# Kernel tuning notes

Hardware: AMD Instinct MI355X
Metric: run time of the kernel (lower is better)

Reference implementation:

```python
import jax, jax.numpy as jnp
import numpy as np

# dims
B, S, LC, K, CE, L, WE, H = 64, 512, 16, 3, 10, 32, 200, 200
V, A, T = 50000, 128, 64
LP = LC + K - 1  # padded word length (pad_word adds (K-1)/2 on each side)
D_IN = WE + L    # LSTM input dim = 232


def setup_inputs() -> dict:
    key = jax.random.key(0)
    ks = jax.random.split(key, 16)
    f = lambda k, shp: jax.random.normal(k, shp, dtype=jnp.float32) * 0.05
    return {
        "char_ids": jax.random.randint(ks[0], (B, S, LP), 0, A),
        "word_ids": jax.random.randint(ks[1], (B, S), 0, V),
        "word_emb": f(ks[2], (V, WE)),
        "char_emb": f(ks[3], (A, CE)),
        "conv_w": f(ks[4], (L, K * CE)),   # Conv1d(1, l, K*CE) == linear 30->32
        "conv_b": f(ks[5], (L,)),
        "w_ih_f": f(ks[6], (4 * H, D_IN)),
        "w_hh_f": f(ks[7], (4 * H, H)),
        "b_ih_f": f(ks[8], (4 * H,)),
        "b_hh_f": f(ks[9], (4 * H,)),
        "w_ih_b": f(ks[10], (4 * H, D_IN)),
        "w_hh_b": f(ks[11], (4 * H, H)),
        "b_ih_b": f(ks[12], (4 * H,)),
        "b_hh_b": f(ks[13], (4 * H,)),
        "out_w": f(ks[14], (T, 2 * H)),
        "out_b": f(ks[15], (T,)),
    }


def _lstm(x, w_ih, w_hh, b_ih, b_hh, reverse):
    # x: [S, B, D]; PyTorch gate order i, f, g, o
    def step(carry, x_t):
        h, c = carry
        g = x_t @ w_ih.T + b_ih + h @ w_hh.T + b_hh
        i, f, gg, o = jnp.split(g, 4, axis=-1)
        c = jax.nn.sigmoid(f) * c + jax.nn.sigmoid(i) * jnp.tanh(gg)
        h = jax.nn.sigmoid(o) * jnp.tanh(c)
        return (h, c), h

    b = x.shape[1]
    init = (jnp.zeros((b, H), x.dtype), jnp.zeros((b, H), x.dtype))
    _, hs = jax.lax.scan(step, init, x, reverse=reverse)
    return hs  # [S, B, H]


def reference(char_ids, word_ids, word_emb, char_emb, conv_w, conv_b,
              w_ih_f, w_hh_f, b_ih_f, b_hh_f,
              w_ih_b, w_hh_b, b_ih_b, b_hh_b,
              out_w, out_b):
    # per-word char CNN + max-pool, fully batched over (B, S, windows)
    ce = char_emb[char_ids]                                    # [B,S,LP,CE]
    # sliding K-char windows, flattened to K*CE (== original x_hat construction)
    win = jnp.concatenate([ce[:, :, k:k + LC] for k in range(K)], axis=-1)  # [B,S,LC,K*CE]
    phi = jnp.einsum('bswd,ld->bswl', win, conv_w) + conv_b    # tiny conv == linear
    char_repr = phi.max(axis=2)                                # max-pool over positions -> [B,S,L]

    combined = jnp.concatenate([word_emb[word_ids], char_repr], axis=-1)  # [B,S,232]
    x = combined.reshape(S, B, D_IN)  # faithful to original .view (reshape, not transpose)

    hf = _lstm(x, w_ih_f, w_hh_f, b_ih_f, b_hh_f, reverse=False)
    hb = _lstm(x, w_ih_b, w_hh_b, b_ih_b, b_hh_b, reverse=True)
    lstm_out = jnp.concatenate([hf, hb], axis=-1)              # [S,B,2H]  (dropout: eval mode)

    tag_space = lstm_out.reshape(B, S, 2 * H) @ out_w.T + out_b  # faithful .view back
    return jax.nn.log_softmax(tag_space, axis=1)  # original normalizes over dim=1 (seq axis)
```

## Files before the change

kernel.cpp:

```cpp
#include <hip/hip_runtime.h>
#include <hip/hip_bf16.h>
#include <math.h>

constexpr int B_ = 64, S_ = 512, LP_ = 18, CE_ = 10, LF_ = 32;
constexpr int WE_ = 200, H_ = 200, T_ = 64;
constexpr int N_ = B_ * S_;
constexpr int KP_ = 256;
constexpr int G4_ = 800;
constexpr int NG_ = 1600;
constexpr float L2E_ = 1.4426950408889634f;

typedef short short8 __attribute__((ext_vector_type(8)));
typedef float f32x4 __attribute__((ext_vector_type(4)));

__device__ __forceinline__ ushort bf16bits(float v) {
  return __bfloat16_as_ushort(__float2bfloat16(v));
}
__device__ __forceinline__ float bf2f(ushort u) {
  return __uint_as_float(((uint)u) << 16);
}
__device__ __forceinline__ float exp2fast(float x) {
#if defined(__has_builtin)
#if __has_builtin(__builtin_amdgcn_exp2f)
  return __builtin_amdgcn_exp2f(x);
#else
  float r; asm("v_exp_f32 %0, %1" : "=v"(r) : "v"(x)); return r;
#endif
#else
  float r; asm("v_exp_f32 %0, %1" : "=v"(r) : "v"(x)); return r;
#endif
}
__device__ __forceinline__ float sig2(float y) {
  return __builtin_amdgcn_rcpf(1.f + exp2fast(-y));
}

__global__ __launch_bounds__(256) void k_build_x(
    const int* __restrict__ char_ids, const int* __restrict__ word_ids,
    const float* __restrict__ word_emb, const float* __restrict__ char_emb,
    const float* __restrict__ conv_w, const float* __restrict__ conv_b,
    ushort* __restrict__ Xb)
{
  __shared__ float ce[4][LP_ * CE_];
  const int wave = threadIdx.x >> 6, lane = threadIdx.x & 63;
  const int n = blockIdx.x * 4 + wave;

  for (int i = lane; i < LP_ * CE_; i += 64) {
    int c = char_ids[n * LP_ + i / CE_];
    ce[wave][i] = char_emb[c * CE_ + (i % CE_)];
  }
  const float* we = word_emb + (size_t)word_ids[n] * WE_;
  ushort* xr = Xb + (size_t)n * KP_;
  for (int i = lane; i < WE_; i += 64) xr[i] = bf16bits(we[i]);
  if (lane < KP_ - WE_ - LF_) xr[WE_ + LF_ + lane] = 0;
  __syncthreads();

  const int f = lane & 31, half = lane >> 5;
  float cw[30];
  #pragma unroll
  for (int i = 0; i < 30; ++i) cw[i] = conv_w[f * 30 + i];
  float m = -1e30f;
  for (int w = half * 8; w < half * 8 + 8; ++w) {
    float acc = 0.f;
    #pragma unroll
    for (int i = 0; i < 30; ++i) acc += ce[wave][w * CE_ + i] * cw[i];
    m = fmaxf(m, acc);
  }
  m = fmaxf(m, __shfl_xor(m, 32));
  if (half == 0) xr[WE_ + f] = bf16bits(m + conv_b[f]);
}

__global__ __launch_bounds__(64) void k_pack_w(
    const float* __restrict__ w_ih_f, const float* __restrict__ w_ih_b,
    const float* __restrict__ b_ih_f, const float* __restrict__ b_hh_f,
    const float* __restrict__ b_ih_b, const float* __restrict__ b_hh_b,
    ushort* __restrict__ Wb, float* __restrict__ biasc)
{
  const int r = blockIdx.x;
  const int rl = r < G4_ ? r : r - G4_;
  const int gate = rl / 200;
  const float sc = (gate == 2) ? 2.f * L2E_ : L2E_;
  const float* src = r < G4_ ? w_ih_f + (size_t)rl * 232 : w_ih_b + (size_t)rl * 232;
  for (int c = threadIdx.x; c < KP_; c += 64)
    Wb[(size_t)r * KP_ + c] = (c < 232) ? bf16bits(src[c] * sc) : (ushort)0;
  if (threadIdx.x == 0)
    biasc[r] = sc * (r < G4_ ? (b_ih_f[rl] + b_hh_f[rl]) : (b_ih_b[rl] + b_hh_b[rl]));
}

__global__ __launch_bounds__(256) void k_gemm_proj(
    const ushort* __restrict__ Xb, const ushort* __restrict__ Wb,
    const float* __restrict__ biasc, ushort* __restrict__ Gc)
{
  __shared__ __align__(16) char smem[65536];
  const int tid = threadIdx.x;
  const int lane = tid & 63, w = tid >> 6;
  const int wr = w >> 1, wc = w & 1;
  const int rowbase = blockIdx.y * 64, colbase = blockIdx.x * 64;

  const char* Ag = (const char*)(Xb + (size_t)rowbase * KP_);
  const char* Bg = (const char*)(Wb + (size_t)colbase * KP_);
  #pragma unroll
  for (int it = 0; it < 8; ++it) {
    int slot = it * 256 + tid;
    int row = slot >> 5, c16 = slot & 31;
    int src = row * 512 + c16 * 16;
    int dst = row * 512 + ((c16 * 16) ^ ((row & 7) << 4));
    *(short8*)(smem + dst) = *(const short8*)(Ag + src);
    *(short8*)(smem + 32768 + dst) = *(const short8*)(Bg + src);
  }
  __syncthreads();

  f32x4 acc[2][2] = {};
  #pragma unroll
  for (int kk = 0; kk < 8; ++kk) {
    const int kb = kk * 64 + (lane >> 4) * 16;
    short8 a[2], b[2];
    #pragma unroll
    for (int m = 0; m < 2; ++m) {
      int ar = wr * 32 + m * 16 + (lane & 15);
      a[m] = *(const short8*)(smem + ar * 512 + (kb ^ ((ar & 7) << 4)));
      int bc = wc * 32 + m * 16 + (lane & 15);
      b[m] = *(const short8*)(smem + 32768 + bc * 512 + (kb ^ ((bc & 7) << 4)));
    }
    #pragma unroll
    for (int m = 0; m < 2; ++m)
      #pragma unroll
      for (int n = 0; n < 2; ++n)
        acc[m][n] = __builtin_amdgcn_mfma_f32_16x16x32_bf16(a[m], b[n], acc[m][n], 0, 0, 0);
  }
  __syncthreads();

  float* Cs = (float*)smem;
  #pragma unroll
  for (int m = 0; m < 2; ++m)
    #pragma unroll
    for (int n = 0; n < 2; ++n)
      #pragma unroll
      for (int i = 0; i < 4; ++i) {
        int r = wr * 32 + m * 16 + (lane >> 4) * 4 + i;
        int c = wc * 32 + n * 16 + (lane & 15);
        Cs[r * 65 + c] = acc[m][n][i];
      }
  __syncthreads();

  const int r = tid >> 2, cg = (tid & 3) * 16;
  ushort ob[16];
  #pragma unroll
  for (int j = 0; j < 16; ++j)
    ob[j] = bf16bits(Cs[r * 65 + cg + j] + biasc[colbase + cg + j]);
  ushort* dst = Gc + (size_t)(rowbase + r) * NG_ + colbase + cg;
  *(short8*)(dst) = *(short8*)(ob);
  *(short8*)(dst + 8) = *(short8*)(ob + 8);
}

__global__ __launch_bounds__(1024) void k_lstm(
    const ushort* __restrict__ Gc,
    const float* __restrict__ w_hh_f, const float* __restrict__ w_hh_b,
    ushort* __restrict__ hf, ushort* __restrict__ hb)
{
  __shared__ ushort h_lds[2][16][232];
  __shared__ __align__(16) char wlds45[2][65536];
  __shared__ __align__(16) char wlds6[17408];

  const int tid = threadIdx.x;
  const int lane = tid & 63, w = tid >> 6;
  const int lo = lane & 15, hi = lane >> 4;
  const int dir = blockIdx.x >> 3, grp = blockIdx.x & 7;
  const float* Whh = dir ? w_hh_b : w_hh_f;
  ushort* hout = dir ? hb : hf;

  for (int i = tid; i < 2 * 16 * 232; i += 1024) ((ushort*)h_lds)[i] = 0;
  if (tid < 256) ((uint*)(wlds6 + 16384))[tid] = 0;

  const int s = w;
  const int off = s < 12 ? 12 * s : 144 + 16 * (s - 12);
  const int cnt = s < 12 ? 12 : 16;
  const int rl  = min(cnt, 200 - off);

  short8 wreg[4][4];
  #pragma unroll
  for (int g = 0; g < 4; ++g) {
    const float sc = (g == 2) ? 2.f * L2E_ : L2E_;
    const float* wr = Whh + (size_t)(g * 200 + off + lo) * 200;
    const bool rowok = lo < rl;
    const int gid = s * 4 + g;
    #pragma unroll
    for (int kt = 0; kt < 7; ++kt) {
      const int k0 = kt * 32 + hi * 8;
      float v[8];
      if (rowok && k0 < 200) {
        float4 p0 = *(const float4*)(wr + k0);
        float4 p1 = *(const float4*)(wr + k0 + 4);
        v[0] = p0.x; v[1] = p0.y; v[2] = p0.z; v[3] = p0.w;
        v[4] = p1.x; v[5] = p1.y; v[6] = p1.z; v[7] = p1.w;
      } else {
        #pragma unroll
        for (int j = 0; j < 8; ++j) v[j] = 0.f;
      }
      short8 fr;
      #pragma unroll
      for (int j = 0; j < 8; ++j) fr[j] = (short)bf16bits(v[j] * sc);
      if (kt < 4) wreg[g][kt] = fr;
      else if (kt < 6) *(short8*)(wlds45[kt - 4] + gid * 1024 + lane * 16) = fr;
      else if (hi == 0) *(short8*)(wlds6 + gid * 256 + lo * 16) = fr;
    }
  }

  float c_[4] = {};

  const int rowsel = lo & 7;
  const int step0 = dir ? (S_ - 1) : 0;
  const ushort* gpp = Gc + (size_t)(step0 * 64 + grp * 8 + rowsel) * NG_ + dir * G4_ + off + hi * 4;
  ushort* sp = hout + (size_t)(step0 * 64 + grp * 8 + lo) * H_ + off + hi * 4;
  const ptrdiff_t gstep = (dir ? -64 : 64) * (ptrdiff_t)NG_;
  const ptrdiff_t hstep = (dir ? -64 : 64) * (ptrdiff_t)H_;
  const bool storemask = (lo < 8) && (hi * 4 < rl);
  const bool ldsmask   = (lo < 8) && (hi * 4 < rl);

  const char* base45a = wlds45[0] + s * 4096 + lane * 16;
  const char* base45b = wlds45[1] + s * 4096 + lane * 16;
  const char* base6   = wlds6 + ((hi == 0) ? (s * 1024 + lo * 16) : (16384 + lo * 16));

  __syncthreads();

  #pragma unroll 2
  for (int t = 0; t < S_; ++t) {
    const ushort (*HR)[232] = h_lds[t & 1];
    ushort (*HW)[232] = h_lds[(t & 1) ^ 1];

    uint2 pre[4];
    #pragma unroll
    for (int g = 0; g < 4; ++g)
      pre[g] = *(const uint2*)(gpp + g * 200);

    __builtin_amdgcn_s_setprio(1);
    f32x4 acc[4] = {};
    const char* hrow = (const char*)HR + lo * 464 + hi * 16;
    #pragma unroll
    for (int kt = 0; kt < 7; ++kt) {
      short8 hfr = *(const short8*)(hrow + kt * 64);
      if (kt < 4) {
        #pragma unroll
        for (int g = 0; g < 4; ++g)
          acc[g] = __builtin_amdgcn_mfma_f32_16x16x32_bf16(wreg[g][kt], hfr, acc[g], 0, 0, 0);
      } else if (kt == 4) {
        #pragma unroll
        for (int g = 0; g < 4; ++g) {
          short8 wk = *(const short8*)(base45a + g * 1024);
          acc[g] = __builtin_amdgcn_mfma_f32_16x16x32_bf16(wk, hfr, acc[g], 0, 0, 0);
        }
      } else if (kt == 5) {
        #pragma unroll
        for (int g = 0; g < 4; ++g) {
          short8 wk = *(const short8*)(base45b + g * 1024);
          acc[g] = __builtin_amdgcn_mfma_f32_16x16x32_bf16(wk, hfr, acc[g], 0, 0, 0);
        }
      } else {
        #pragma unroll
        for (int g = 0; g < 4; ++g) {
          short8 wk = *(const short8*)(base6 + g * 256);
          acc[g] = __builtin_amdgcn_mfma_f32_16x16x32_bf16(wk, hfr, acc[g], 0, 0, 0);
        }
      }
    }
    __builtin_amdgcn_s_setprio(0);

    const uint2 pi = pre[0], pf = pre[1], pg = pre[2], po = pre[3];
    float hv[4];
    #pragma unroll
    for (int i = 0; i < 4; ++i) {
      const uint wi = (i < 2) ? pi.x : pi.y;
      const uint wf = (i < 2) ? pf.x : pf.y;
      const uint wg = (i < 2) ? pg.x : pg.y;
      const uint wo = (i < 2) ? po.x : po.y;
      const int sh = (i & 1) * 16;
      float gi = acc[0][i] + bf2f((ushort)(wi >> sh));
      float gf = acc[1][i] + bf2f((ushort)(wf >> sh));
      float gg = acc[2][i] + bf2f((ushort)(wg >> sh));
      float go = acc[3][i] + bf2f((ushort)(wo >> sh));
      float si = sig2(gi);
      float sf = sig2(gf);
      float so = sig2(go);
      float tg = 2.f * sig2(gg) - 1.f;
      float cn = sf * c_[i] + si * tg;
      c_[i] = cn;
      float tc = 2.f * sig2(cn * (2.f * L2E_)) - 1.f;
      hv[i] = so * tc;
    }
    uint2 pk;
    pk.x = (uint)bf16bits(hv[0]) | ((uint)bf16bits(hv[1]) << 16);
    pk.y = (uint)bf16bits(hv[2]) | ((uint)bf16bits(hv[3]) << 16);
    if (ldsmask)
      *(uint2*)((char*)HW + lo * 464 + off * 2 + hi * 8) = pk;

    __syncthreads();

    if (storemask) *(uint2*)sp = pk;
    sp += hstep;
    gpp += gstep;
  }
}

__global__ __launch_bounds__(256) void k_out(
    const ushort* __restrict__ hf, const ushort* __restrict__ hb,
    const float* __restrict__ out_w, const float* __restrict__ out_b,
    float* __restrict__ tag)
{
  const int m = threadIdx.x >> 3;
  const int tg = threadIdx.x & 7;
  const int n = blockIdx.x * 32 + m;
  const ushort* hfp = hf + (size_t)n * H_;
  const ushort* hbp = hb + (size_t)n * H_;
  float acc[8];
  #pragma unroll
  for (int q = 0; q < 8; ++q) acc[q] = out_b[tg + 8 * q];
  for (int k = 0; k < H_ / 4; ++k) {
    uint2 hv = *(const uint2*)(hfp + k * 4);
    float x0 = bf2f((ushort)hv.x), x1 = bf2f((ushort)(hv.x >> 16));
    float x2 = bf2f((ushort)hv.y), x3 = bf2f((ushort)(hv.y >> 16));
    #pragma unroll
    for (int q = 0; q < 8; ++q) {
      float4 w = ((const float4*)(out_w + (size_t)(tg + 8 * q) * 2 * H_))[k];
      acc[q] += x0 * w.x + x1 * w.y + x2 * w.z + x3 * w.w;
    }
  }
  for (int k = 0; k < H_ / 4; ++k) {
    uint2 hv = *(const uint2*)(hbp + k * 4);
    float x0 = bf2f((ushort)hv.x), x1 = bf2f((ushort)(hv.x >> 16));
    float x2 = bf2f((ushort)hv.y), x3 = bf2f((ushort)(hv.y >> 16));
    #pragma unroll
    for (int q = 0; q < 8; ++q) {
      float4 w = ((const float4*)(out_w + (size_t)(tg + 8 * q) * 2 * H_ + H_))[k];
      acc[q] += x0 * w.x + x1 * w.y + x2 * w.z + x3 * w.w;
    }
  }
  #pragma unroll
  for (int q = 0; q < 8; ++q) tag[(size_t)n * T_ + tg + 8 * q] = acc[q];
}

__global__ __launch_bounds__(256) void k_lsm(
    const float* __restrict__ tag, float* __restrict__ out)
{
  __shared__ float red[4][T_];
  __shared__ float lse[T_];
  const int b = blockIdx.x;
  const int tt = threadIdx.x & 63, ch = threadIdx.x >> 6;
  const float* tb = tag + (size_t)b * S_ * T_;

  float m = -1e30f;
  for (int s = ch * 128; s < ch * 128 + 128; ++s) m = fmaxf(m, tb[s * T_ + tt]);
  red[ch][tt] = m;
  __syncthreads();
  if (ch == 0)
    lse[tt] = fmaxf(fmaxf(red[0][tt], red[1][tt]), fmaxf(red[2][tt], red[3][tt]));
  __syncthreads();
  m = lse[tt];
  float sum = 0.f;
  for (int s = ch * 128; s < ch * 128 + 128; ++s) sum += __expf(tb[s * T_ + tt] - m);
  __syncthreads();
  red[ch][tt] = sum;
  __syncthreads();
  if (ch == 0)
    lse[tt] = m + logf(red[0][tt] + red[1][tt] + red[2][tt] + red[3][tt]);
  __syncthreads();
  const float l = lse[tt];
  float* ob = out + (size_t)b * S_ * T_;
  for (int s = ch * 128; s < ch * 128 + 128; ++s) ob[s * T_ + tt] = tb[s * T_ + tt] - l;
}

extern "C" void kernel_launch(void* const* d_in, const int* in_sizes, int n_in,
                              void* d_out, int out_size, void* d_ws, size_t ws_size,
                              hipStream_t stream) {
  const int*   char_ids = (const int*)d_in[0];
  const int*   word_ids = (const int*)d_in[1];
  const float* word_emb = (const float*)d_in[2];
  const float* char_emb = (const float*)d_in[3];
  const float* conv_w   = (const float*)d_in[4];
  const float* conv_b   = (const float*)d_in[5];
  const float* w_ih_f   = (const float*)d_in[6];
  const float* w_hh_f   = (const float*)d_in[7];
  const float* b_ih_f   = (const float*)d_in[8];
  const float* b_hh_f   = (const float*)d_in[9];
  const float* w_ih_b   = (const float*)d_in[10];
  const float* w_hh_b   = (const float*)d_in[11];
  const float* b_ih_b   = (const float*)d_in[12];
  const float* b_hh_b   = (const float*)d_in[13];
  const float* out_w    = (const float*)d_in[14];
  const float* out_b    = (const float*)d_in[15];

  char* ws = (char*)d_ws;
  ushort* Xb    = (ushort*)(ws);
  ushort* Wb    = (ushort*)(ws + 16777216);
  float*  biasc = (float*) (ws + 17596416);
  ushort* Gc    = (ushort*)(ws + 18422016);
  ushort* hf    = (ushort*)(ws + 123279616);
  ushort* hb    = (ushort*)(ws + 136386816);
  float*  tag   = (float*) (ws + 149494016);

  hipLaunchKernelGGL(k_build_x, dim3(N_ / 4), dim3(256), 0, stream,
                     char_ids, word_ids, word_emb, char_emb, conv_w, conv_b, Xb);
  hipLaunchKernelGGL(k_pack_w, dim3(NG_), dim3(64), 0, stream,
                     w_ih_f, w_ih_b, b_ih_f, b_hh_f, b_ih_b, b_hh_b, Wb, biasc);
  hipLaunchKernelGGL(k_gemm_proj, dim3(NG_ / 64, N_ / 64), dim3(256), 0, stream,
                     Xb, Wb, biasc, Gc);
  hipLaunchKernelGGL(k_lstm, dim3(16), dim3(1024), 0, stream, Gc, w_hh_f, w_hh_b, hf, hb);
  hipLaunchKernelGGL(k_out, dim3(N_ / 32), dim3(256), 0, stream, hf, hb, out_w, out_b, tag);
  hipLaunchKernelGGL(k_lsm, dim3(B_), dim3(256), 0, stream, tag, (float*)d_out);
}
```

Baseline: 1.615 ms.

## Prefetch next-step gate preactivations and use LDS-only barrier in LSTM loop

The recurrent loop now software-pipelines the global loads of the precomputed input-gate values, issuing step t+1's loads during step t through ping-pong register buffers. The per-step __syncthreads is replaced by an explicit lgkmcnt(0) wait plus s_barrier, so the barrier no longer drains the outstanding global prefetch. This aims to hide global-memory latency on the serial critical path of the recurrence. The last iteration prefetches one step past the sequence end, reading out-of-range memory whose values go unused. The exp2 helper is also simplified to always use inline v_exp_f32 asm.

Result: slower. 2.217 ms (+37.3%).

```diff
diff --git a/kernel.cpp b/kernel.cpp
--- a/kernel.cpp
+++ b/kernel.cpp
@@ -20,15 +20,7 @@
   return __uint_as_float(((uint)u) << 16);
 }
 __device__ __forceinline__ float exp2fast(float x) {
-#if defined(__has_builtin)
-#if __has_builtin(__builtin_amdgcn_exp2f)
-  return __builtin_amdgcn_exp2f(x);
-#else
   float r; asm("v_exp_f32 %0, %1" : "=v"(r) : "v"(x)); return r;
-#endif
-#else
-  float r; asm("v_exp_f32 %0, %1" : "=v"(r) : "v"(x)); return r;
-#endif
 }
 __device__ __forceinline__ float sig2(float y) {
   return __builtin_amdgcn_rcpf(1.f + exp2fast(-y));
@@ -220,17 +212,17 @@
   const char* base45b = wlds45[1] + s * 4096 + lane * 16;
   const char* base6   = wlds6 + ((hi == 0) ? (s * 1024 + lo * 16) : (16384 + lo * 16));
 
-  __syncthreads();
-
-  #pragma unroll 2
-  for (int t = 0; t < S_; ++t) {
-    const ushort (*HR)[232] = h_lds[t & 1];
-    ushort (*HW)[232] = h_lds[(t & 1) ^ 1];
-
-    uint2 pre[4];
-    #pragma unroll
-    for (int g = 0; g < 4; ++g)
-      pre[g] = *(const uint2*)(gpp + g * 200);
+  uint2 preA[4], preB[4];
+  #pragma unroll
+  for (int g = 0; g < 4; ++g) preA[g] = *(const uint2*)(gpp + g * 200);
+  gpp += gstep;
+
+  __syncthreads();
+
+  auto lstm_step = [&](const ushort (*HR)[232], ushort (*HW)[232],
+                       uint2 (&pc)[4], uint2 (&pn)[4]) {
+    #pragma unroll
+    for (int g = 0; g < 4; ++g) pn[g] = *(const uint2*)(gpp + g * 200);
 
     __builtin_amdgcn_s_setprio(1);
     f32x4 acc[4] = {};
@@ -264,7 +256,7 @@
     }
     __builtin_amdgcn_s_setprio(0);
 
-    const uint2 pi = pre[0], pf = pre[1], pg = pre[2], po = pre[3];
+    const uint2 pi = pc[0], pf = pc[1], pg = pc[2], po = pc[3];
     float hv[4];
     #pragma unroll
     for (int i = 0; i < 4; ++i) {
@@ -292,11 +284,19 @@
     if (ldsmask)
       *(uint2*)((char*)HW + lo * 464 + off * 2 + hi * 8) = pk;
 
-    __syncthreads();
+    asm volatile("s_waitcnt lgkmcnt(0)" ::: "memory");
+    __builtin_amdgcn_sched_barrier(0);
+    __builtin_amdgcn_s_barrier();
+    __builtin_amdgcn_sched_barrier(0);
 
     if (storemask) *(uint2*)sp = pk;
     sp += hstep;
     gpp += gstep;
+  };
+
+  for (int tt = 0; tt < S_; tt += 2) {
+    lstm_step(h_lds[0], h_lds[1], preA, preB);
+    lstm_step(h_lds[1], h_lds[0], preB, preA);
   }
 }
 
```
